# Kernel optimization log

Hardware: AMD Instinct MI355X
Metric: run time of the kernel (lower is better)

## Reference

```python
import jax, jax.numpy as jnp
import numpy as np

EMBED_DIM = 1024
NUM_HEADS = 16
HEAD_DIM = EMBED_DIM // NUM_HEADS


def setup_inputs() -> dict:
    key = jax.random.key(0)
    ks = jax.random.split(key, 9)
    B, S, D = 2, 2048, EMBED_DIM
    scale = 1.0 / np.sqrt(D)
    x = jax.random.normal(ks[0], (B, S, D), dtype=jnp.float32)
    wq = jax.random.normal(ks[1], (D, D), dtype=jnp.float32) * scale
    bq = jax.random.normal(ks[2], (D,), dtype=jnp.float32) * 0.02
    wk = jax.random.normal(ks[3], (D, D), dtype=jnp.float32) * scale
    bk = jax.random.normal(ks[4], (D,), dtype=jnp.float32) * 0.02
    wv = jax.random.normal(ks[5], (D, D), dtype=jnp.float32) * scale
    bv = jax.random.normal(ks[6], (D,), dtype=jnp.float32) * 0.02
    wo = jax.random.normal(ks[7], (D, D), dtype=jnp.float32) * scale
    bo = jax.random.normal(ks[8], (D,), dtype=jnp.float32) * 0.02
    return {"x": x, "wq": wq, "bq": bq, "wk": wk, "bk": bk,
            "wv": wv, "bv": bv, "wo": wo, "bo": bo}


def reference(x, wq, bq, wk, bk, wv, bv, wo, bo):
    B, S, D = x.shape
    H, Hd = NUM_HEADS, HEAD_DIM
    # separate QKV linears (weights stored [in, out] so x @ w)
    q = (x @ wq + bq).reshape(B, S, H, Hd).transpose(0, 2, 1, 3)  # [B,H,S,Hd]
    k = (x @ wk + bk).reshape(B, S, H, Hd).transpose(0, 2, 1, 3)
    v = (x @ wv + bv).reshape(B, S, H, Hd).transpose(0, 2, 1, 3)
    scores = jnp.einsum('bhqd,bhkd->bhqk', q, k) / jnp.sqrt(jnp.float32(Hd))
    attn = jax.nn.softmax(scores, axis=-1)
    context = jnp.einsum('bhqk,bhkd->bhqd', attn, v)
    context = context.transpose(0, 2, 1, 3).reshape(B, S, D)
    return context @ wo + bo
```

## Files before the change

kernel.cpp:

```cpp
#include <hip/hip_runtime.h>
#include <cstdint>
#include <cstddef>


typedef float floatx4 __attribute__((ext_vector_type(4)));
typedef __bf16 bf16x8 __attribute__((ext_vector_type(8)));
union ABFrag { bf16x8 v; uint4 q; unsigned short u[8]; unsigned int w[4]; };

__device__ __forceinline__ unsigned short f2bf(float f) {
    unsigned int u = __builtin_bit_cast(unsigned int, f);
    return (unsigned short)((u + 0x7FFFu + ((u >> 16) & 1u)) >> 16);
}

__device__ __forceinline__ unsigned int cvtpk(float lo, float hi) {
    unsigned int r;
    asm("v_cvt_pk_bf16_f32 %0, %1, %2" : "=v"(r) : "v"(lo), "v"(hi));
    return r;
}

#if __has_builtin(__builtin_amdgcn_exp2f)
#define EXP2F(x) __builtin_amdgcn_exp2f(x)
#else
#define EXP2F(x) exp2f(x)
#endif

__device__ __forceinline__ void glds16(const void* g, void* l) {
    __builtin_amdgcn_global_load_lds(
        (const __attribute__((address_space(1))) unsigned int*)(uintptr_t)g,
        (__attribute__((address_space(3))) unsigned int*)(unsigned int)(uintptr_t)l,
        16, 0, 0);
}

__global__ void convert_fused_kernel(const float* __restrict__ x,
                                     const float* __restrict__ w0,
                                     const float* __restrict__ w1,
                                     const float* __restrict__ w2,
                                     const float* __restrict__ w3,
                                     unsigned short* __restrict__ xb,
                                     unsigned short* __restrict__ wT) {
    const int tid = threadIdx.x;
    if (blockIdx.x < 2048) {
        int i = (blockIdx.x * 256 + tid) * 8;
        float4 a = *(const float4*)(x + i);
        float4 b = *(const float4*)(x + i + 4);
        union { unsigned short u[8]; uint4 q; } o;
        o.u[0] = f2bf(a.x); o.u[1] = f2bf(a.y); o.u[2] = f2bf(a.z); o.u[3] = f2bf(a.w);
        o.u[4] = f2bf(b.x); o.u[5] = f2bf(b.y); o.u[6] = f2bf(b.z); o.u[7] = f2bf(b.w);
        *(uint4*)(xb + i) = o.q;
        return;
    }
    __shared__ unsigned short t[32][40];
    const int wi = blockIdx.x - 2048;
    const int z  = wi >> 10;
    const int rem = wi & 1023;
    const int k0 = (rem >> 5) * 32, n0 = (rem & 31) * 32;
    const float* w = (z == 0) ? w0 : (z == 1) ? w1 : (z == 2) ? w2 : w3;
    unsigned short* dst = wT + (size_t)z * 1024 * 1024;
    {
        int ry = tid >> 3, cx = (tid & 7) * 4;
        float4 v = *(const float4*)(w + (size_t)(k0 + ry) * 1024 + n0 + cx);
        t[cx + 0][ry] = f2bf(v.x); t[cx + 1][ry] = f2bf(v.y);
        t[cx + 2][ry] = f2bf(v.z); t[cx + 3][ry] = f2bf(v.w);
    }
    __syncthreads();
    int n = tid >> 3, kc = (tid & 7) * 4;
    *(uint2*)(dst + (size_t)(n0 + n) * 1024 + k0 + kc) = *(const uint2*)&t[n][kc];
}

template<int KIND>
__launch_bounds__(256, (KIND == 0) ? 2 : 4)
__global__ void gemm_kernel(const unsigned short* __restrict__ A,
                            const unsigned short* __restrict__ wT,
                            const float* __restrict__ bias0,
                            const float* __restrict__ bias1,
                            const float* __restrict__ bias2,
                            void* __restrict__ out0,
                            void* __restrict__ out1,
                            void* __restrict__ out2)
{
    constexpr int BM = 128;
    constexpr int BN = (KIND == 1) ? 64 : 128;
    constexpr int NI = BM / 32;
    constexpr int NJ = BN / 32;

    __shared__ unsigned short a_s[BM * 32];
    __shared__ unsigned short b_s[BN * 32];

    int bx, by, bz;
    if constexpr (KIND == 0) {
        int lin = blockIdx.x + (blockIdx.y << 3) + (blockIdx.z << 8);
        int swz = (lin & 7) * 96 + (lin >> 3);
        bx = swz & 7;
        int rem = swz >> 3;
        by = rem & 31;
        bz = rem >> 5;
    } else {
        int lin = blockIdx.x + (blockIdx.y << 4);
        int swz = ((lin & 7) << 6) + (lin >> 3);
        bx = swz & 15;
        by = swz >> 4;
        bz = 0;
    }

    const int tid  = threadIdx.x;
    const int wid  = tid >> 6;
    const int lane = tid & 63;
    const int quad = lane >> 4;
    const int l15  = lane & 15;
    const int wm   = (wid >> 1) * (BM / 2);
    const int wn   = (wid & 1) * (BN / 2);
    const int m0   = by * BM;
    const int n0   = bx * BN;

    const unsigned short* Bt = (KIND == 0) ? wT + (size_t)bz * (1024 * 1024) : wT;
    const float* bias = (KIND == 0)
        ? (bz == 0 ? bias0 : bz == 1 ? bias1 : bias2) : bias0;

    const int sr = lane >> 2;
    const int sc = (lane & 3) * 8;
    const unsigned short* gA = A + (size_t)(m0 + wid * 32 + sr) * 1024 + sc;
    const unsigned short* gB = Bt + (size_t)(n0 + wid * (BN / 4) + sr) * 1024 + sc;
    unsigned short* lA = a_s + wid * 1024;
    unsigned short* lB = b_s + wid * (BN / 4) * 32;

    floatx4 acc[NI][NJ];
    #pragma unroll
    for (int i = 0; i < NI; i++)
        #pragma unroll
        for (int j = 0; j < NJ; j++)
            acc[i][j] = floatx4{0.f, 0.f, 0.f, 0.f};

    for (int k0 = 0; k0 < 1024; k0 += 32) {
        __syncthreads();
        glds16(gA + k0, lA);
        glds16(gA + k0 + 16 * 1024, lA + 512);
        glds16(gB + k0, lB);
        if constexpr (KIND == 0) glds16(gB + k0 + 16 * 1024, lB + 512);
        __syncthreads();

        ABFrag af[NI], bf4[NJ];
        #pragma unroll
        for (int i = 0; i < NI; i++)
            af[i].q = *(const uint4*)(a_s + (wm + i * 16 + l15) * 32 + quad * 8);
        #pragma unroll
        for (int j = 0; j < NJ; j++)
            bf4[j].q = *(const uint4*)(b_s + (wn + j * 16 + l15) * 32 + quad * 8);
        #pragma unroll
        for (int i = 0; i < NI; i++)
            #pragma unroll
            for (int j = 0; j < NJ; j++)
                acc[i][j] = __builtin_amdgcn_mfma_f32_16x16x32_bf16(
                    af[i].v, bf4[j].v, acc[i][j], 0, 0, 0);
    }

    if constexpr (KIND == 1) {
        float* out = (float*)out0;
        #pragma unroll
        for (int j = 0; j < NJ; j++) {
            int gn = n0 + wn + j * 16 + l15;
            float bval = bias[gn];
            #pragma unroll
            for (int i = 0; i < NI; i++)
                #pragma unroll
                for (int r = 0; r < 4; r++) {
                    int gm = m0 + wm + i * 16 + quad * 4 + r;
                    out[(size_t)gm * 1024 + gn] = acc[i][j][r] + bval;
                }
        }
    } else {
        if (bz == 0) {
            const float SCQ = 0.125f * 1.44269504088896f;
            unsigned short* out = (unsigned short*)out0;
            #pragma unroll
            for (int j = 0; j < NJ; j++) {
                int gn = n0 + wn + j * 16 + l15;
                float bval = bias[gn];
                int h = gn >> 6, d = gn & 63;
                #pragma unroll
                for (int i = 0; i < NI; i++)
                    #pragma unroll
                    for (int r = 0; r < 4; r++) {
                        int gm = m0 + wm + i * 16 + quad * 4 + r;
                        int b = gm >> 11, s = gm & 2047;
                        out[(((size_t)(b * 16 + h) * 2048 + s) << 6) + d] =
                            f2bf((acc[i][j][r] + bval) * SCQ);
                    }
            }
        } else if (bz == 1) {
            unsigned short* out = (unsigned short*)out1;
            #pragma unroll
            for (int j = 0; j < NJ; j++) {
                int gn = n0 + wn + j * 16 + l15;
                float bval = bias[gn];
                int h = gn >> 6, d = gn & 63;
                int dg = d >> 3, dl = d & 7;
                #pragma unroll
                for (int i = 0; i < NI; i++)
                    #pragma unroll
                    for (int r = 0; r < 4; r++) {
                        int gm = m0 + wm + i * 16 + quad * 4 + r;
                        int b = gm >> 11, s = gm & 2047;
                        int dphys = ((dg ^ (s & 7)) << 3) | dl;
                        out[(((size_t)(b * 16 + h) * 2048 + s) << 6) + dphys] =
                            f2bf(acc[i][j][r] + bval);
                    }
            }
        } else {
            __shared__ unsigned short t_s[128][72];
            unsigned short* out = (unsigned short*)out2;
            const int n    = tid >> 1;
            const int gph  = tid & 1;
            const int bh = (m0 >> 11) * 16 + ((n0 + n) >> 6);
            const int d  = (n0 + n) & 63;
            const int dmask  = d & 7;
            const int chunk0 = (m0 & 2047) >> 6;
            #pragma unroll
            for (int mh = 0; mh < 2; mh++) {
                if ((wid >> 1) == mh) {
                    #pragma unroll
                    for (int j = 0; j < NJ; j++) {
                        int nl = wn + j * 16 + l15;
                        float bval = bias[n0 + nl];
                        #pragma unroll
                        for (int i = 0; i < NI; i++)
                            #pragma unroll
                            for (int r = 0; r < 4; r++)
                                t_s[nl][i * 16 + quad * 4 + r] =
                                    f2bf(acc[i][j][r] + bval);
                    }
                }
                __syncthreads();
                {
                    unsigned short* dstb =
                        out + ((size_t)(bh * 32 + chunk0 + mh) * 64 + d) * 64;
                    const unsigned short* src = &t_s[n][0];
                    #pragma unroll
                    for (int g = 0; g < 4; g++) {
                        int gp = gph * 4 + g;
                        int u1 = 32 * (gp >> 2) + 4 * (gp & 3);
                        uint2 lo = *(const uint2*)(src + u1);
                        uint2 hi = *(const uint2*)(src + u1 + 16);
                        unsigned short* dq = dstb + ((gp ^ dmask) << 3);
                        *(uint2*)dq       = lo;
                        *(uint2*)(dq + 4) = hi;
                    }
                }
                __syncthreads();
            }
        }
    }
}

__launch_bounds__(512, 2)
__global__ void attn_kernel(const unsigned short* __restrict__ Q,
                            const unsigned short* __restrict__ K,
                            const unsigned short* __restrict__ Vt,
                            unsigned short* __restrict__ ctx)
{
    __shared__ unsigned short smem[2][2][2][4096];

    const int lin = blockIdx.x + (blockIdx.y << 3);
    const int swz = ((lin & 7) << 5) + (lin >> 3);
    const int qx  = swz & 7;
    const int bh  = swz >> 3;

    const int tid  = threadIdx.x;
    const int wid  = tid >> 6;
    const int kh   = wid >> 2;
    const int wq   = wid & 3;
    const int lane = tid & 63;
    const int quad = lane >> 4;
    const int l15  = lane & 15;
    const int xr   = l15 & 7;

    const unsigned short* Qh = Q + (size_t)bh * (2048 * 64);
    const char* Kc = (const char*)(K  + (size_t)bh * (2048 * 64)) + (size_t)kh * (16 * 8192);
    const char* Vc = (const char*)(Vt + (size_t)bh * (2048 * 64)) + (size_t)kh * (16 * 8192);
    const int q0 = qx * 256 + wq * 64;

    ABFrag qf[4][2];
    #pragma unroll
    for (int jq = 0; jq < 4; jq++)
        #pragma unroll
        for (int s = 0; s < 2; s++)
            qf[jq][s].q = *(const uint4*)(Qh + (size_t)(q0 + jq * 16 + l15) * 64
                                          + s * 32 + quad * 8);

    int kcol[2];
    kcol[0] = ((quad    ) ^ xr) << 3;
    kcol[1] = ((quad + 4) ^ xr) << 3;

    floatx4 acc[4][4];
    #pragma unroll
    for (int i = 0; i < 4; i++)
        #pragma unroll
        for (int jq = 0; jq < 4; jq++)
            acc[i][jq] = floatx4{0.f, 0.f, 0.f, 0.f};
    float lrun[4] = {0.f, 0.f, 0.f, 0.f};

    auto stage = [&](int c, int b) {
        const char* gk = Kc + (size_t)c * 8192 + wq * 2048 + lane * 16;
        char* lk = (char*)&smem[b][kh][0][0] + wq * 2048;
        glds16(gk,        lk);
        glds16(gk + 1024, lk + 1024);
        const char* gv = Vc + (size_t)c * 8192 + wq * 2048 + lane * 16;
        char* lv = (char*)&smem[b][kh][1][0] + wq * 2048;
        glds16(gv,        lv);
        glds16(gv + 1024, lv + 1024);
    };

    stage(0, 0);

    for (int c = 0; c < 16; ++c) {
        const int b = c & 1;
        __syncthreads();
        if (c + 1 < 16) stage(c + 1, b ^ 1);

        const unsigned short* ks = &smem[b][kh][0][0];
        const unsigned short* vs = &smem[b][kh][1][0];

        floatx4 st[4][4];
        #pragma unroll
        for (int kt = 0; kt < 4; kt++) {
            ABFrag k0, k1;
            const unsigned short* kr = ks + (kt * 16 + l15) * 64;
            k0.q = *(const uint4*)(kr + kcol[0]);
            k1.q = *(const uint4*)(kr + kcol[1]);
            #pragma unroll
            for (int jq = 0; jq < 4; jq++) {
                floatx4 t = floatx4{0.f, 0.f, 0.f, 0.f};
                t = __builtin_amdgcn_mfma_f32_16x16x32_bf16(k0.v, qf[jq][0].v, t, 0, 0, 0);
                t = __builtin_amdgcn_mfma_f32_16x16x32_bf16(k1.v, qf[jq][1].v, t, 0, 0, 0);
                st[kt][jq] = t;
            }
        }

        unsigned int pk[4][4][2];
        #pragma unroll
        for (int jq = 0; jq < 4; jq++) {
            float ls = 0.f;
            #pragma unroll
            for (int kt = 0; kt < 4; kt++) {
                #pragma unroll
                for (int t2 = 0; t2 < 2; t2++) {
                    float p0 = EXP2F(st[kt][jq][2 * t2 + 0]);
                    float p1 = EXP2F(st[kt][jq][2 * t2 + 1]);
                    ls += p0 + p1;
                    pk[kt][jq][t2] = cvtpk(p0, p1);
                }
            }
            lrun[jq] += ls;
        }

        #pragma unroll
        for (int s2 = 0; s2 < 2; s2++) {
            ABFrag pf[4];
            #pragma unroll
            for (int jq = 0; jq < 4; jq++) {
                pf[jq].w[0] = pk[2 * s2 + 0][jq][0];
                pf[jq].w[1] = pk[2 * s2 + 0][jq][1];
                pf[jq].w[2] = pk[2 * s2 + 1][jq][0];
                pf[jq].w[3] = pk[2 * s2 + 1][jq][1];
            }
            #pragma unroll
            for (int i = 0; i < 4; i++) {
                ABFrag vf;
                vf.q = *(const uint4*)(vs + (i * 16 + l15) * 64 + kcol[s2]);
                #pragma unroll
                for (int jq = 0; jq < 4; jq++)
                    acc[i][jq] = __builtin_amdgcn_mfma_f32_16x16x32_bf16(
                        vf.v, pf[jq].v, acc[i][jq], 0, 0, 0);
            }
        }
    }

    __syncthreads();
    float* sf = (float*)&smem[0][0][0][0];
    float* myp = sf + (size_t)(wq * 64 + lane) * 36;
    if (kh) {
        #pragma unroll
        for (int i = 0; i < 2; i++)
            #pragma unroll
            for (int jq = 0; jq < 4; jq++)
                *(floatx4*)(myp + (i * 4 + jq) * 4) = acc[i][jq];
        myp[32] = lrun[0];
        myp[33] = lrun[1];
    }
    __syncthreads();
    if (!kh) {
        #pragma unroll
        for (int i = 0; i < 2; i++)
            #pragma unroll
            for (int jq = 0; jq < 4; jq++)
                acc[i][jq] += *(const floatx4*)(myp + (i * 4 + jq) * 4);
        lrun[0] += myp[32];
        lrun[1] += myp[33];
    }
    __syncthreads();
    if (kh) {
        #pragma unroll
        for (int i = 2; i < 4; i++)
            #pragma unroll
            for (int jq = 0; jq < 4; jq++)
                *(floatx4*)(myp + ((i - 2) * 4 + jq) * 4) = acc[i][jq];
        myp[32] = lrun[2];
        myp[33] = lrun[3];
    }
    __syncthreads();
    if (!kh) {
        #pragma unroll
        for (int i = 2; i < 4; i++)
            #pragma unroll
            for (int jq = 0; jq < 4; jq++)
                acc[i][jq] += *(const floatx4*)(myp + ((i - 2) * 4 + jq) * 4);
        lrun[2] += myp[32];
        lrun[3] += myp[33];

        const int b_ = bh >> 4, h = bh & 15;
        #pragma unroll
        for (int jq = 0; jq < 4; jq++) {
            float s = lrun[jq];
            s += __shfl_xor(s, 16, 64);
            s += __shfl_xor(s, 32, 64);
            float inv = 1.0f / s;
            int q = q0 + jq * 16 + l15;
            size_t base = (size_t)(b_ * 2048 + q) * 1024 + h * 64;
            #pragma unroll
            for (int i = 0; i < 4; i++) {
                float v0 = acc[i][jq][0] * inv, v1 = acc[i][jq][1] * inv;
                float v2 = acc[i][jq][2] * inv, v3 = acc[i][jq][3] * inv;
                uint2 w2 = make_uint2(cvtpk(v0, v1), cvtpk(v2, v3));
                *(uint2*)(ctx + base + i * 16 + quad * 4) = w2;
            }
        }
    }
}

extern "C" void kernel_launch(void* const* d_in, const int* in_sizes, int n_in,
                              void* d_out, int out_size, void* d_ws, size_t ws_size,
                              hipStream_t stream)
{
    const float* x  = (const float*)d_in[0];
    const float* wq = (const float*)d_in[1];
    const float* bq = (const float*)d_in[2];
    const float* wk = (const float*)d_in[3];
    const float* bk = (const float*)d_in[4];
    const float* wv = (const float*)d_in[5];
    const float* bv = (const float*)d_in[6];
    const float* wo = (const float*)d_in[7];
    const float* bo = (const float*)d_in[8];

    const size_t NE = (size_t)4096 * 1024;
    unsigned short* xb  = (unsigned short*)d_ws;
    unsigned short* wT  = xb  + NE;
    unsigned short* qb  = wT  + NE;
    unsigned short* kb  = qb  + NE;
    unsigned short* vtb = kb  + NE;
    unsigned short* ctx = vtb + NE;

    hipLaunchKernelGGL(convert_fused_kernel, dim3(6144), dim3(256), 0, stream,
                       x, wq, wk, wv, wo, xb, wT);
    hipLaunchKernelGGL((gemm_kernel<0>), dim3(8, 32, 3), dim3(256), 0, stream,
                       xb, wT, bq, bk, bv, (void*)qb, (void*)kb, (void*)vtb);
    hipLaunchKernelGGL(attn_kernel, dim3(8, 32), dim3(512), 0, stream, qb, kb, vtb, ctx);
    hipLaunchKernelGGL((gemm_kernel<1>), dim3(16, 32), dim3(256), 0, stream,
                       ctx, wT + 3 * NE / 4, bo, nullptr, nullptr, d_out, nullptr, nullptr);
}
```

Before: 182.8 us.

## Double-buffer GEMM shared-memory tiles and shrink output-projection tile to 64x64

Both GEMM kernels now use two LDS buffers. The global-to-LDS load for the next K step is issued before the MFMA work on the current step, and the loop needs one barrier per iteration instead of two. This is meant to hide global load latency behind compute. The output-projection GEMM also moves from 128x64 to 64x64 tiles, doubling its grid to 1024 blocks with a matching swizzle, and both kinds use a minimum of 2 blocks in the launch bounds. The cost is double the LDS use per block, which may limit occupancy, plus smaller output tiles with less data reuse.

```diff
diff --git a/kernel.cpp b/kernel.cpp
--- a/kernel.cpp
+++ b/kernel.cpp
@@ -68,7 +68,7 @@
 }
 
 template<int KIND>
-__launch_bounds__(256, (KIND == 0) ? 2 : 4)
+__launch_bounds__(256, 2)
 __global__ void gemm_kernel(const unsigned short* __restrict__ A,
                             const unsigned short* __restrict__ wT,
                             const float* __restrict__ bias0,
@@ -78,13 +78,13 @@
                             void* __restrict__ out1,
                             void* __restrict__ out2)
 {
-    constexpr int BM = 128;
+    constexpr int BM = (KIND == 1) ? 64 : 128;
     constexpr int BN = (KIND == 1) ? 64 : 128;
     constexpr int NI = BM / 32;
     constexpr int NJ = BN / 32;
 
-    __shared__ unsigned short a_s[BM * 32];
-    __shared__ unsigned short b_s[BN * 32];
+    __shared__ unsigned short a_s[2][BM * 32];
+    __shared__ unsigned short b_s[2][BN * 32];
 
     int bx, by, bz;
     if constexpr (KIND == 0) {
@@ -96,7 +96,7 @@
         bz = rem >> 5;
     } else {
         int lin = blockIdx.x + (blockIdx.y << 4);
-        int swz = ((lin & 7) << 6) + (lin >> 3);
+        int swz = ((lin & 7) << 7) + (lin >> 3);
         bx = swz & 15;
         by = swz >> 4;
         bz = 0;
@@ -118,10 +118,18 @@
 
     const int sr = lane >> 2;
     const int sc = (lane & 3) * 8;
-    const unsigned short* gA = A + (size_t)(m0 + wid * 32 + sr) * 1024 + sc;
+    const unsigned short* gA = A + (size_t)(m0 + wid * (BM / 4) + sr) * 1024 + sc;
     const unsigned short* gB = Bt + (size_t)(n0 + wid * (BN / 4) + sr) * 1024 + sc;
-    unsigned short* lA = a_s + wid * 1024;
-    unsigned short* lB = b_s + wid * (BN / 4) * 32;
+    const int laOff = wid * (BM / 4) * 32;
+    const int lbOff = wid * (BN / 4) * 32;
+
+    auto stage = [&](int t, int buf) {
+        const int k0 = t * 32;
+        glds16(gA + k0, a_s[buf] + laOff);
+        if constexpr (KIND == 0) glds16(gA + k0 + 16 * 1024, a_s[buf] + laOff + 512);
+        glds16(gB + k0, b_s[buf] + lbOff);
+        if constexpr (KIND == 0) glds16(gB + k0 + 16 * 1024, b_s[buf] + lbOff + 512);
+    };
 
     floatx4 acc[NI][NJ];
     #pragma unroll
@@ -130,21 +138,20 @@
         for (int j = 0; j < NJ; j++)
             acc[i][j] = floatx4{0.f, 0.f, 0.f, 0.f};
 
-    for (int k0 = 0; k0 < 1024; k0 += 32) {
+    stage(0, 0);
+
+    for (int t = 0; t < 32; ++t) {
+        const int b = t & 1;
         __syncthreads();
-        glds16(gA + k0, lA);
-        glds16(gA + k0 + 16 * 1024, lA + 512);
-        glds16(gB + k0, lB);
-        if constexpr (KIND == 0) glds16(gB + k0 + 16 * 1024, lB + 512);
-        __syncthreads();
+        if (t + 1 < 32) stage(t + 1, b ^ 1);
 
         ABFrag af[NI], bf4[NJ];
         #pragma unroll
         for (int i = 0; i < NI; i++)
-            af[i].q = *(const uint4*)(a_s + (wm + i * 16 + l15) * 32 + quad * 8);
+            af[i].q = *(const uint4*)(a_s[b] + (wm + i * 16 + l15) * 32 + quad * 8);
         #pragma unroll
         for (int j = 0; j < NJ; j++)
-            bf4[j].q = *(const uint4*)(b_s + (wn + j * 16 + l15) * 32 + quad * 8);
+            bf4[j].q = *(const uint4*)(b_s[b] + (wn + j * 16 + l15) * 32 + quad * 8);
         #pragma unroll
         for (int i = 0; i < NI; i++)
             #pragma unroll
@@ -463,6 +470,6 @@
     hipLaunchKernelGGL((gemm_kernel<0>), dim3(8, 32, 3), dim3(256), 0, stream,
                        xb, wT, bq, bk, bv, (void*)qb, (void*)kb, (void*)vtb);
     hipLaunchKernelGGL(attn_kernel, dim3(8, 32), dim3(512), 0, stream, qb, kb, vtb, ctx);
-    hipLaunchKernelGGL((gemm_kernel<1>), dim3(16, 32), dim3(256), 0, stream,
+    hipLaunchKernelGGL((gemm_kernel<1>), dim3(16, 64), dim3(256), 0, stream,
                        ctx, wT + 3 * NE / 4, bo, nullptr, nullptr, d_out, nullptr, nullptr);
 }
```

Measured after the change: 179.9 us. About the same (-1.6%).
